# Optimization experiments

Hardware: AMD Instinct MI355X
Metric: run time of the kernel (lower is better)

The kernel has to match this reference:

```python
import jax, jax.numpy as jnp
import numpy as np

LOG_STD2 = float(np.log(0.001))  # matches nn.init posterior_W_u/v fill, unused: params are random here


def _mvg_layer(x, M, u, v, eps):
    # append ones column (bias trick): [B, in] -> [B, in+1]
    x1 = jnp.concatenate([x, jnp.ones((x.shape[0], 1), x.dtype)], axis=1)
    # W = M + diag(exp(.5u)) @ eps @ diag(exp(.5v))  ==  M + row/col scaled eps
    W = M + jnp.exp(0.5 * u)[:, None] * eps * jnp.exp(0.5 * v)[None, :]
    return x1 @ W


def setup_inputs() -> dict:
    key = jax.random.key(0)
    ks = jax.random.split(key, 17)
    dims = [(2049, 4096), (4097, 4096), (4097, 4096), (4097, 2048)]
    inp = {"x": jax.random.normal(ks[0], (8192, 2048), dtype=jnp.float32)}
    ki = 1
    for i, (fin, fout) in enumerate(dims):
        inp[f"M{i}"] = jax.random.normal(ks[ki], (fin, fout), dtype=jnp.float32) * 0.001; ki += 1
        inp[f"u{i}"] = jax.random.normal(ks[ki], (fin,), dtype=jnp.float32) + LOG_STD2; ki += 1
        inp[f"v{i}"] = jax.random.normal(ks[ki], (fout,), dtype=jnp.float32) + LOG_STD2; ki += 1
        inp[f"eps{i}"] = jax.random.normal(ks[ki], (fin, fout), dtype=jnp.float32); ki += 1
    return inp


def reference(x, M0, u0, v0, eps0, M1, u1, v1, eps1, M2, u2, v2, eps2, M3, u3, v3, eps3):
    h = _mvg_layer(x, M0, u0, v0, eps0)
    h = _mvg_layer(jax.nn.relu(h), M1, u1, v1, eps1)
    h = _mvg_layer(jax.nn.relu(h), M2, u2, v2, eps2)
    h = _mvg_layer(jax.nn.relu(h), M3, u3, v3, eps3)
    return h
```

## Files before the change

### kernel.cpp

```cpp
#include <hip/hip_runtime.h>
#include <cstdint>
#include <cstddef>

typedef __bf16 bf16_t;
typedef __attribute__((ext_vector_type(8))) __bf16 bf16x8;
typedef __attribute__((ext_vector_type(4))) __bf16 bf16x4;
typedef __attribute__((ext_vector_type(16))) float floatx16;

#define SB0 __builtin_amdgcn_sched_barrier(0)
#define LGKM(N)                                             \
  do {                                                      \
    asm volatile("s_waitcnt lgkmcnt(" #N ")" ::: "memory"); \
    SB0;                                                    \
  } while (0)

__device__ __forceinline__ void cp16(const void* g, void* l) {
  __builtin_amdgcn_global_load_lds(
      (const __attribute__((address_space(1))) void*)(uintptr_t)g,
      (__attribute__((address_space(3))) void*)(uintptr_t)l, 16, 0, 0);
}

__device__ __forceinline__ void stage_half(const bf16_t* p, int K, char* dst,
                                           int tid) {
  cp16(p, dst + tid * 16);
  cp16(p + (size_t)128 * K, dst + 8192 + tid * 16);
}

struct PrepArgs {
  const float* x;
  bf16_t* xb;
  const float* M[4];
  const float* u[4];
  const float* v[4];
  const float* e[4];
  bf16_t* Wt[4];
  float* bias[4];
};

__global__ __launch_bounds__(256) void prep_all(PrepArgs a) {
  __shared__ float tile[32][33];
  const int tx = threadIdx.x, ty = threadIdx.y;
  const int tid = ty * 32 + tx;
  int bid = blockIdx.x;

  if (bid < 16384) {
    const int i = bid * 256 + tid;
    float4 f = ((const float4*)a.x)[i];
    bf16x4 o;
    o[0] = (bf16_t)f.x; o[1] = (bf16_t)f.y; o[2] = (bf16_t)f.z; o[3] = (bf16_t)f.w;
    ((bf16x4*)a.xb)[i] = o;
    return;
  }
  bid -= 16384;

  if (bid >= 49152) {
    const int b = bid - 49152;
    int layer, base;
    if (b < 16) { layer = 0; base = b; }
    else if (b < 32) { layer = 1; base = b - 16; }
    else if (b < 48) { layer = 2; base = b - 32; }
    else { layer = 3; base = b - 48; }
    const int K = (layer == 0) ? 2048 : 4096;
    const int N = (layer == 3) ? 2048 : 4096;
    const int n = base * 256 + tid;
    if (n < N) {
      const size_t idx = (size_t)K * N + n;
      a.bias[layer][n] = a.M[layer][idx] +
                         __expf(0.5f * a.u[layer][K]) * a.e[layer][idx] *
                             __expf(0.5f * a.v[layer][n]);
    }
    return;
  }

  int layer, nbx, kby, K, N;
  if (bid < 8192) { layer = 0; K = 2048; N = 4096; nbx = bid & 127; kby = bid >> 7; }
  else if (bid < 24576) { layer = 1; K = 4096; N = 4096; int b = bid - 8192; nbx = b & 127; kby = b >> 7; }
  else if (bid < 40960) { layer = 2; K = 4096; N = 4096; int b = bid - 24576; nbx = b & 127; kby = b >> 7; }
  else { layer = 3; K = 4096; N = 2048; int b = bid - 40960; nbx = b & 63; kby = b >> 6; }
  const float* M = a.M[layer];
  const float* u = a.u[layer];
  const float* v = a.v[layer];
  const float* eps = a.e[layer];
  bf16_t* Wt = a.Wt[layer];
  const int nb = nbx * 32, kb = kby * 32;
  const float sv = __expf(0.5f * v[nb + tx]);
#pragma unroll
  for (int r = 0; r < 4; ++r) {
    const int k = kb + ty + 8 * r;
    const float su = __expf(0.5f * u[k]);
    const size_t idx = (size_t)k * N + nb + tx;
    tile[ty + 8 * r][tx] = M[idx] + su * eps[idx] * sv;
  }
  __syncthreads();
#pragma unroll
  for (int r = 0; r < 4; ++r) {
    const int n = nb + ty + 8 * r;
    Wt[(size_t)n * K + kb + tx] = (bf16_t)tile[tx][ty + 8 * r];
  }
}

__device__ __forceinline__ void rd6(const char* HA, const char* HB, int aoff,
                                    int boff, bf16x8 (&af)[4], bf16x8 (&bb)[2]) {
  bb[0] = *(const bf16x8*)(HB + boff);
  bb[1] = *(const bf16x8*)(HB + boff + 2048);
  af[0] = *(const bf16x8*)(HA + aoff);
  af[1] = *(const bf16x8*)(HA + aoff + 2048);
  af[2] = *(const bf16x8*)(HA + aoff + 4096);
  af[3] = *(const bf16x8*)(HA + aoff + 6144);
}

__device__ __forceinline__ void mf8(const bf16x8 (&af)[4], const bf16x8 (&bb)[2],
                                    floatx16 (&acc)[4][2]) {
  __builtin_amdgcn_s_setprio(1);
#pragma unroll
  for (int mb = 0; mb < 4; ++mb)
#pragma unroll
    for (int nb = 0; nb < 2; ++nb)
      acc[mb][nb] = __builtin_amdgcn_mfma_f32_32x32x16_bf16(
          bb[nb], af[mb], acc[mb][nb], 0, 0, 0);
  __builtin_amdgcn_s_setprio(0);
}

template <int CURB>
__device__ __forceinline__ void ktile(int t, int NT, int K, const bf16_t* gA,
                                      const bf16_t* gB, char* lds, int tid,
                                      int aoff0, int aoff1, int boff0, int boff1,
                                      floatx16 (&acc)[4][2]) {
  constexpr int curO = CURB * 65536;
  constexpr int nxtO = (CURB ^ 1) * 65536;
  const char* A0 = lds + curO;
  const char* A1 = lds + curO + 16384;
  const char* B0 = lds + curO + 32768;
  const char* B1h = lds + curO + 49152;
  bf16x8 afX[4], bbX[2], afY[4], bbY[2], afZ[4], bbZ[2];

  if (t + 1 < NT) {
    stage_half(gA + (size_t)(t + 1) * 64 + 32, K, lds + nxtO + 16384, tid);
    stage_half(gB + (size_t)(t + 1) * 64 + 32, K, lds + nxtO + 49152, tid);
  }
  rd6(A0, B0, aoff0, boff0, afX, bbX);
  SB0;
  rd6(A0, B0, aoff1, boff1, afY, bbY);
  SB0;
  LGKM(6);
  mf8(afX, bbX, acc);
  rd6(A1, B1h, aoff0, boff0, afZ, bbZ);
  SB0;
  rd6(A1, B1h, aoff1, boff1, afX, bbX);
  SB0;
  LGKM(12);
  mf8(afY, bbY, acc);
  SB0;
  __builtin_amdgcn_s_barrier();
  SB0;
  if (t + 2 < NT) {
    stage_half(gA + (size_t)(t + 2) * 64, K, lds + curO, tid);
    stage_half(gB + (size_t)(t + 2) * 64, K, lds + curO + 32768, tid);
  }
  LGKM(6);
  mf8(afZ, bbZ, acc);
  LGKM(0);
  mf8(afX, bbX, acc);
  SB0;
  if (t + 2 < NT) {
    asm volatile("s_waitcnt vmcnt(4)" ::: "memory");
  } else if (t + 1 < NT) {
    asm volatile("s_waitcnt vmcnt(0)" ::: "memory");
  }
  SB0;
  __builtin_amdgcn_s_barrier();
  SB0;
}

template <int EPI>
__global__ __launch_bounds__(512, 2) void gemm256(
    const bf16_t* __restrict__ A, const bf16_t* __restrict__ Bt,
    const float* __restrict__ bias, void* __restrict__ Cout, int N, int K) {
  extern __shared__ char lds[];
  const int tid = threadIdx.x;
  const int lane = tid & 63;
  const int wave = tid >> 6;
  const int wm = (wave >> 2) * 128;
  const int wn = (wave & 3) * 64;

  const int l31 = lane & 31;
  const int kh = lane >> 5;
  const int lA = wm + l31;
  const int lB = wn + l31;
  const int xA = (lA >> 1) & 3;
  const int xB = (lB >> 1) & 3;
  const int aoff0 = lA * 64 + ((kh ^ xA) << 4);
  const int aoff1 = lA * 64 + (((2 + kh) ^ xA) << 4);
  const int boff0 = lB * 64 + ((kh ^ xB) << 4);
  const int boff1 = lB * 64 + (((2 + kh) ^ xB) << 4);

  const int gx = gridDim.x;
  int id = blockIdx.y * gx + blockIdx.x;
  const int cpx = (gx * (int)gridDim.y) >> 3;
  id = (id & 7) * cpx + (id >> 3);
  const int bm = (id / gx) * 256;
  const int bn = (id % gx) * 256;

  const int srow = tid >> 2;
  const int ss8 = ((tid & 3) ^ ((tid >> 3) & 3)) * 8;
  const bf16_t* gA = A + (size_t)(bm + srow) * K + ss8;
  const bf16_t* gB = Bt + (size_t)(bn + srow) * K + ss8;

  const int NT = K >> 6;

  floatx16 acc[4][2] = {};

  stage_half(gA, K, lds + 0, tid);
  stage_half(gA + 32, K, lds + 16384, tid);
  stage_half(gB, K, lds + 32768, tid);
  stage_half(gB + 32, K, lds + 49152, tid);
  stage_half(gA + 64, K, lds + 65536, tid);
  stage_half(gB + 64, K, lds + 65536 + 32768, tid);
  asm volatile("s_waitcnt vmcnt(4)" ::: "memory");
  __builtin_amdgcn_s_barrier();
  SB0;

  for (int t = 0; t < NT; t += 2) {
    ktile<0>(t, NT, K, gA, gB, lds, tid, aoff0, aoff1, boff0, boff1, acc);
    ktile<1>(t + 1, NT, K, gA, gB, lds, tid, aoff0, aoff1, boff0, boff1, acc);
  }

  const int m0 = bm + wm + l31;
  const int kh4 = kh * 4;
#pragma unroll
  for (int nb = 0; nb < 2; ++nb) {
#pragma unroll
    for (int q = 0; q < 4; ++q) {
      const int col = bn + wn + nb * 32 + q * 8 + kh4;
      const float4 b4 = *(const float4*)&bias[col];
#pragma unroll
      for (int mb = 0; mb < 4; ++mb) {
        float x0 = acc[mb][nb][q * 4 + 0] + b4.x;
        float x1 = acc[mb][nb][q * 4 + 1] + b4.y;
        float x2 = acc[mb][nb][q * 4 + 2] + b4.z;
        float x3 = acc[mb][nb][q * 4 + 3] + b4.w;
        const size_t idx = (size_t)(m0 + mb * 32) * N + col;
        if (EPI == 0) {
          x0 = fmaxf(x0, 0.f);
          x1 = fmaxf(x1, 0.f);
          x2 = fmaxf(x2, 0.f);
          x3 = fmaxf(x3, 0.f);
          bf16x4 o;
          o[0] = (bf16_t)x0; o[1] = (bf16_t)x1; o[2] = (bf16_t)x2; o[3] = (bf16_t)x3;
          *(bf16x4*)((bf16_t*)Cout + idx) = o;
        } else {
          *(float4*)((float*)Cout + idx) = make_float4(x0, x1, x2, x3);
        }
      }
    }
  }
}

extern "C" void kernel_launch(void* const* d_in, const int* in_sizes, int n_in,
                              void* d_out, int out_size, void* d_ws, size_t ws_size,
                              hipStream_t stream) {
  const float* x = (const float*)d_in[0];
  const float *Mm[4], *uu[4], *vv[4], *ee[4];
  for (int i = 0; i < 4; ++i) {
    Mm[i] = (const float*)d_in[1 + 4 * i];
    uu[i] = (const float*)d_in[2 + 4 * i];
    vv[i] = (const float*)d_in[3 + 4 * i];
    ee[i] = (const float*)d_in[4 + 4 * i];
  }

  char* ws = (char*)d_ws;
  bf16_t* Wt0 = (bf16_t*)ws;
  bf16_t* Wt1 = (bf16_t*)(ws + 16777216);
  bf16_t* Wt2 = (bf16_t*)(ws + 16777216 + 33554432);
  bf16_t* Wt3 = (bf16_t*)(ws + 16777216 + 2u * 33554432);
  char* bptr = ws + 2u * 16777216 + 2u * 33554432;
  float* bias0 = (float*)(bptr);
  float* bias1 = (float*)(bptr + 16384);
  float* bias2 = (float*)(bptr + 32768);
  float* bias3 = (float*)(bptr + 49152);
  char* act = bptr + 65536;
  bf16_t* hA = (bf16_t*)act;
  bf16_t* hB = (bf16_t*)(act + 67108864);
  bf16_t* xb = (bf16_t*)d_out;

  static bool attr_set = false;
  if (!attr_set) {
    (void)hipFuncSetAttribute(reinterpret_cast<const void*>(&gemm256<0>),
                              hipFuncAttributeMaxDynamicSharedMemorySize, 131072);
    (void)hipFuncSetAttribute(reinterpret_cast<const void*>(&gemm256<1>),
                              hipFuncAttributeMaxDynamicSharedMemorySize, 131072);
    attr_set = true;
  }

  PrepArgs pa;
  pa.x = x;
  pa.xb = xb;
  for (int i = 0; i < 4; ++i) {
    pa.M[i] = Mm[i]; pa.u[i] = uu[i]; pa.v[i] = vv[i]; pa.e[i] = ee[i];
  }
  pa.Wt[0] = Wt0; pa.Wt[1] = Wt1; pa.Wt[2] = Wt2; pa.Wt[3] = Wt3;
  pa.bias[0] = bias0; pa.bias[1] = bias1; pa.bias[2] = bias2; pa.bias[3] = bias3;
  prep_all<<<16384 + 49152 + 56, dim3(32, 8), 0, stream>>>(pa);

  gemm256<0><<<dim3(16, 32), 512, 131072, stream>>>(xb, Wt0, bias0, hA, 4096, 2048);
  gemm256<0><<<dim3(16, 32), 512, 131072, stream>>>(hA, Wt1, bias1, hB, 4096, 4096);
  gemm256<0><<<dim3(16, 32), 512, 131072, stream>>>(hB, Wt2, bias2, hA, 4096, 4096);
  gemm256<1><<<dim3(8, 32), 512, 131072, stream>>>(hA, Wt3, bias3, d_out, 2048, 4096);
}
```

Measured before the change: 1.268 ms.

## Switch GEMM to 16x16x32 MFMA with simplified full-tile prefetch pipeline

Replaces the 32x32x16 bf16 MFMA tiling (4x2 accumulators per wave) with 16x16x32 MFMAs over an 8x4 accumulator grid, with new LDS swizzled offsets and a matching epilogue. The K-tile pipeline now prefetches the whole next tile (both halves) at the top of each step and waits for it at the end. The old split-half staging interleaved with compute is dropped. Waves in the second half start on the other 32-wide K half to spread LDS bank traffic, and per-fragment lgkmcnt waits let MFMAs start as A fragments arrive. This trades the deeper staggered overlap for simpler scheduling and a different MFMA shape.

```diff
diff --git a/kernel.cpp b/kernel.cpp
--- a/kernel.cpp
+++ b/kernel.cpp
@@ -5,7 +5,7 @@
 typedef __bf16 bf16_t;
 typedef __attribute__((ext_vector_type(8))) __bf16 bf16x8;
 typedef __attribute__((ext_vector_type(4))) __bf16 bf16x4;
-typedef __attribute__((ext_vector_type(16))) float floatx16;
+typedef __attribute__((ext_vector_type(4))) float floatx4;
 
 #define SB0 __builtin_amdgcn_sched_barrier(0)
 #define LGKM(N)                                             \
@@ -99,72 +99,86 @@
   }
 }
 
-__device__ __forceinline__ void rd6(const char* HA, const char* HB, int aoff,
-                                    int boff, bf16x8 (&af)[4], bf16x8 (&bb)[2]) {
-  bb[0] = *(const bf16x8*)(HB + boff);
-  bb[1] = *(const bf16x8*)(HB + boff + 2048);
-  af[0] = *(const bf16x8*)(HA + aoff);
-  af[1] = *(const bf16x8*)(HA + aoff + 2048);
-  af[2] = *(const bf16x8*)(HA + aoff + 4096);
-  af[3] = *(const bf16x8*)(HA + aoff + 6144);
-}
-
-__device__ __forceinline__ void mf8(const bf16x8 (&af)[4], const bf16x8 (&bb)[2],
-                                    floatx16 (&acc)[4][2]) {
+__device__ __forceinline__ void half16(const char* Ah, const char* Bh, int aoff,
+                                       int boff, floatx4 (&acc)[8][4]) {
+  bf16x8 af[8], bb[4];
+  af[0] = *(const bf16x8*)(Ah + aoff);
+  bb[0] = *(const bf16x8*)(Bh + boff);
+  bb[1] = *(const bf16x8*)(Bh + boff + 1024);
+  bb[2] = *(const bf16x8*)(Bh + boff + 2048);
+  bb[3] = *(const bf16x8*)(Bh + boff + 3072);
+  SB0;
+  af[1] = *(const bf16x8*)(Ah + aoff + 1024);
+  SB0;
+  af[2] = *(const bf16x8*)(Ah + aoff + 2048);
+  SB0;
+  af[3] = *(const bf16x8*)(Ah + aoff + 3072);
+  SB0;
+  af[4] = *(const bf16x8*)(Ah + aoff + 4096);
+  SB0;
+  af[5] = *(const bf16x8*)(Ah + aoff + 5120);
+  SB0;
+  af[6] = *(const bf16x8*)(Ah + aoff + 6144);
+  SB0;
+  af[7] = *(const bf16x8*)(Ah + aoff + 7168);
+  SB0;
   __builtin_amdgcn_s_setprio(1);
-#pragma unroll
-  for (int mb = 0; mb < 4; ++mb)
-#pragma unroll
-    for (int nb = 0; nb < 2; ++nb)
-      acc[mb][nb] = __builtin_amdgcn_mfma_f32_32x32x16_bf16(
-          bb[nb], af[mb], acc[mb][nb], 0, 0, 0);
+  LGKM(7);
+#pragma unroll
+  for (int j = 0; j < 4; ++j)
+    acc[0][j] = __builtin_amdgcn_mfma_f32_16x16x32_bf16(bb[j], af[0], acc[0][j], 0, 0, 0);
+  LGKM(6);
+#pragma unroll
+  for (int j = 0; j < 4; ++j)
+    acc[1][j] = __builtin_amdgcn_mfma_f32_16x16x32_bf16(bb[j], af[1], acc[1][j], 0, 0, 0);
+  LGKM(5);
+#pragma unroll
+  for (int j = 0; j < 4; ++j)
+    acc[2][j] = __builtin_amdgcn_mfma_f32_16x16x32_bf16(bb[j], af[2], acc[2][j], 0, 0, 0);
+  LGKM(4);
+#pragma unroll
+  for (int j = 0; j < 4; ++j)
+    acc[3][j] = __builtin_amdgcn_mfma_f32_16x16x32_bf16(bb[j], af[3], acc[3][j], 0, 0, 0);
+  LGKM(3);
+#pragma unroll
+  for (int j = 0; j < 4; ++j)
+    acc[4][j] = __builtin_amdgcn_mfma_f32_16x16x32_bf16(bb[j], af[4], acc[4][j], 0, 0, 0);
+  LGKM(2);
+#pragma unroll
+  for (int j = 0; j < 4; ++j)
+    acc[5][j] = __builtin_amdgcn_mfma_f32_16x16x32_bf16(bb[j], af[5], acc[5][j], 0, 0, 0);
+  LGKM(1);
+#pragma unroll
+  for (int j = 0; j < 4; ++j)
+    acc[6][j] = __builtin_amdgcn_mfma_f32_16x16x32_bf16(bb[j], af[6], acc[6][j], 0, 0, 0);
+  LGKM(0);
+#pragma unroll
+  for (int j = 0; j < 4; ++j)
+    acc[7][j] = __builtin_amdgcn_mfma_f32_16x16x32_bf16(bb[j], af[7], acc[7][j], 0, 0, 0);
   __builtin_amdgcn_s_setprio(0);
 }
 
 template <int CURB>
 __device__ __forceinline__ void ktile(int t, int NT, int K, const bf16_t* gA,
                                       const bf16_t* gB, char* lds, int tid,
-                                      int aoff0, int aoff1, int boff0, int boff1,
-                                      floatx16 (&acc)[4][2]) {
+                                      int aoff0, int boff0, int firstO,
+                                      floatx4 (&acc)[8][4]) {
   constexpr int curO = CURB * 65536;
   constexpr int nxtO = (CURB ^ 1) * 65536;
-  const char* A0 = lds + curO;
-  const char* A1 = lds + curO + 16384;
-  const char* B0 = lds + curO + 32768;
-  const char* B1h = lds + curO + 49152;
-  bf16x8 afX[4], bbX[2], afY[4], bbY[2], afZ[4], bbZ[2];
-
   if (t + 1 < NT) {
-    stage_half(gA + (size_t)(t + 1) * 64 + 32, K, lds + nxtO + 16384, tid);
-    stage_half(gB + (size_t)(t + 1) * 64 + 32, K, lds + nxtO + 49152, tid);
-  }
-  rd6(A0, B0, aoff0, boff0, afX, bbX);
-  SB0;
-  rd6(A0, B0, aoff1, boff1, afY, bbY);
-  SB0;
-  LGKM(6);
-  mf8(afX, bbX, acc);
-  rd6(A1, B1h, aoff0, boff0, afZ, bbZ);
-  SB0;
-  rd6(A1, B1h, aoff1, boff1, afX, bbX);
-  SB0;
-  LGKM(12);
-  mf8(afY, bbY, acc);
-  SB0;
-  __builtin_amdgcn_s_barrier();
-  SB0;
-  if (t + 2 < NT) {
-    stage_half(gA + (size_t)(t + 2) * 64, K, lds + curO, tid);
-    stage_half(gB + (size_t)(t + 2) * 64, K, lds + curO + 32768, tid);
-  }
-  LGKM(6);
-  mf8(afZ, bbZ, acc);
-  LGKM(0);
-  mf8(afX, bbX, acc);
-  SB0;
-  if (t + 2 < NT) {
-    asm volatile("s_waitcnt vmcnt(4)" ::: "memory");
-  } else if (t + 1 < NT) {
+    const bf16_t* pa = gA + (size_t)(t + 1) * 64;
+    const bf16_t* pb = gB + (size_t)(t + 1) * 64;
+    stage_half(pa, K, lds + nxtO, tid);
+    stage_half(pa + 32, K, lds + nxtO + 16384, tid);
+    stage_half(pb, K, lds + nxtO + 32768, tid);
+    stage_half(pb + 32, K, lds + nxtO + 49152, tid);
+  }
+  SB0;
+  const int h0 = firstO;
+  const int h1 = 16384 - firstO;
+  half16(lds + curO + h0, lds + curO + 32768 + h0, aoff0, boff0, acc);
+  half16(lds + curO + h1, lds + curO + 32768 + h1, aoff0, boff0, acc);
+  if (t + 1 < NT) {
     asm volatile("s_waitcnt vmcnt(0)" ::: "memory");
   }
   SB0;
@@ -182,17 +196,11 @@
   const int wave = tid >> 6;
   const int wm = (wave >> 2) * 128;
   const int wn = (wave & 3) * 64;
-
-  const int l31 = lane & 31;
-  const int kh = lane >> 5;
-  const int lA = wm + l31;
-  const int lB = wn + l31;
-  const int xA = (lA >> 1) & 3;
-  const int xB = (lB >> 1) & 3;
-  const int aoff0 = lA * 64 + ((kh ^ xA) << 4);
-  const int aoff1 = lA * 64 + (((2 + kh) ^ xA) << 4);
-  const int boff0 = lB * 64 + ((kh ^ xB) << 4);
-  const int boff1 = lB * 64 + (((2 + kh) ^ xB) << 4);
+  const int l15 = lane & 15;
+  const int kqs = ((lane >> 4) ^ ((lane >> 1) & 3)) << 4;
+  const int aoff0 = (wm + l15) * 64 + kqs;
+  const int boff0 = (wn + l15) * 64 + kqs;
+  const int firstO = (wave < 4) ? 0 : 16384;
 
   const int gx = gridDim.x;
   int id = blockIdx.y * gx + blockIdx.x;
@@ -208,49 +216,47 @@
 
   const int NT = K >> 6;
 
-  floatx16 acc[4][2] = {};
+  floatx4 acc[8][4] = {};
 
   stage_half(gA, K, lds + 0, tid);
   stage_half(gA + 32, K, lds + 16384, tid);
   stage_half(gB, K, lds + 32768, tid);
   stage_half(gB + 32, K, lds + 49152, tid);
-  stage_half(gA + 64, K, lds + 65536, tid);
-  stage_half(gB + 64, K, lds + 65536 + 32768, tid);
-  asm volatile("s_waitcnt vmcnt(4)" ::: "memory");
+  asm volatile("s_waitcnt vmcnt(0)" ::: "memory");
   __builtin_amdgcn_s_barrier();
   SB0;
 
   for (int t = 0; t < NT; t += 2) {
-    ktile<0>(t, NT, K, gA, gB, lds, tid, aoff0, aoff1, boff0, boff1, acc);
-    ktile<1>(t + 1, NT, K, gA, gB, lds, tid, aoff0, aoff1, boff0, boff1, acc);
-  }
-
-  const int m0 = bm + wm + l31;
-  const int kh4 = kh * 4;
-#pragma unroll
-  for (int nb = 0; nb < 2; ++nb) {
-#pragma unroll
-    for (int q = 0; q < 4; ++q) {
-      const int col = bn + wn + nb * 32 + q * 8 + kh4;
-      const float4 b4 = *(const float4*)&bias[col];
-#pragma unroll
-      for (int mb = 0; mb < 4; ++mb) {
-        float x0 = acc[mb][nb][q * 4 + 0] + b4.x;
-        float x1 = acc[mb][nb][q * 4 + 1] + b4.y;
-        float x2 = acc[mb][nb][q * 4 + 2] + b4.z;
-        float x3 = acc[mb][nb][q * 4 + 3] + b4.w;
-        const size_t idx = (size_t)(m0 + mb * 32) * N + col;
-        if (EPI == 0) {
-          x0 = fmaxf(x0, 0.f);
-          x1 = fmaxf(x1, 0.f);
-          x2 = fmaxf(x2, 0.f);
-          x3 = fmaxf(x3, 0.f);
-          bf16x4 o;
-          o[0] = (bf16_t)x0; o[1] = (bf16_t)x1; o[2] = (bf16_t)x2; o[3] = (bf16_t)x3;
-          *(bf16x4*)((bf16_t*)Cout + idx) = o;
-        } else {
-          *(float4*)((float*)Cout + idx) = make_float4(x0, x1, x2, x3);
-        }
+    ktile<0>(t, NT, K, gA, gB, lds, tid, aoff0, boff0, firstO, acc);
+    ktile<1>(t + 1, NT, K, gA, gB, lds, tid, aoff0, boff0, firstO, acc);
+  }
+
+  const int kq4 = lane >> 4;
+  const int row00 = bm + wm + l15;
+  const int colq = bn + wn + kq4 * 4;
+  float4 b4[4];
+#pragma unroll
+  for (int j = 0; j < 4; ++j) b4[j] = *(const float4*)&bias[colq + j * 16];
+#pragma unroll
+  for (int i = 0; i < 8; ++i) {
+    const size_t rbase = (size_t)(row00 + i * 16) * N;
+#pragma unroll
+    for (int j = 0; j < 4; ++j) {
+      float x0 = acc[i][j][0] + b4[j].x;
+      float x1 = acc[i][j][1] + b4[j].y;
+      float x2 = acc[i][j][2] + b4[j].z;
+      float x3 = acc[i][j][3] + b4[j].w;
+      if (EPI == 0) {
+        x0 = fmaxf(x0, 0.f);
+        x1 = fmaxf(x1, 0.f);
+        x2 = fmaxf(x2, 0.f);
+        x3 = fmaxf(x3, 0.f);
+        bf16x4 o;
+        o[0] = (bf16_t)x0; o[1] = (bf16_t)x1; o[2] = (bf16_t)x2; o[3] = (bf16_t)x3;
+        *(bf16x4*)((bf16_t*)Cout + rbase + colq + j * 16) = o;
+      } else {
+        float4 o = make_float4(x0, x1, x2, x3);
+        *(float4*)((float*)Cout + rbase + colq + j * 16) = o;
       }
     }
   }
```

Result: slower. 1.326 ms (+4.6%).
